# Kernel tuning notes

Hardware: AMD Instinct MI355X
Metric: run time of the kernel (lower is better)

Reference implementation:

```python
import jax, jax.numpy as jnp
import numpy as np
from jax import lax

B, CIN, COUT, K, L = 128, 8, 64, 33, 4096
STRIDE, PAD = 1, 16
HID, NW = 128, 3  # agent hidden, num wavelet types (morlet, mexhat, laplace)
MEXHAT_NORM = 2.0 / (np.sqrt(3.0) * np.pi ** 0.25)


def setup_inputs() -> dict:
    key = jax.random.key(0)
    ks = jax.random.split(key, 12)
    s = 0.05  # small init scale for agent weights
    return {
        "x": jax.random.normal(ks[0], (B, CIN, L), jnp.float32),
        # torch init: ones; add small noise so per-wavelet scales differ
        "superparams": jnp.ones((COUT, CIN, NW), jnp.float32)
        + 0.1 * jax.random.normal(ks[1], (COUT, CIN, NW), jnp.float32),
        "threshold": jnp.full((COUT,), 0.1, jnp.float32),
        "fw": s * jax.random.normal(ks[2], (2 * CIN, HID), jnp.float32),
        "fb": jnp.zeros((HID,), jnp.float32),
        "vw1": s * jax.random.normal(ks[3], (HID, HID), jnp.float32),
        "vb1": jnp.zeros((HID,), jnp.float32),
        "vw2": s * jax.random.normal(ks[4], (HID, 1), jnp.float32),
        "vb2": jnp.zeros((1,), jnp.float32),
        "aw1": s * jax.random.normal(ks[5], (HID, HID), jnp.float32),
        "ab1": jnp.zeros((HID,), jnp.float32),
        "aw2": s * jax.random.normal(ks[6], (HID, NW), jnp.float32),
        "ab2": jnp.zeros((NW,), jnp.float32),
    }


def _softplus_pos(p):
    return jax.nn.softplus(p) + 1e-6


def _make_kernels(superparams):
    # superparams: [COUT, CIN, NW] -> kernel bank [NW, COUT, CIN, K]
    grid = jnp.arange(-(K // 2), K // 2 + 1, dtype=jnp.float32)  # [K]
    scale = _softplus_pos(superparams)  # [COUT, CIN, NW]
    kernels = []
    for i, name in enumerate(("morlet", "mexhat", "laplace")):
        xi = grid[None, None, :] / scale[:, :, i : i + 1]  # [COUT, CIN, K]
        if name == "morlet":
            ker = jnp.exp(-0.5 * xi * xi) * jnp.cos(5.0 * xi)
        elif name == "mexhat":
            ker = MEXHAT_NORM * (1.0 - xi * xi) * jnp.exp(-0.5 * xi * xi)
        else:  # laplace
            ker = jnp.sign(grid)[None, None, :] * jnp.exp(-jnp.abs(xi))
        ker = ker - ker.mean(axis=-1, keepdims=True)
        ker = ker / (jnp.linalg.norm(ker, axis=-1, keepdims=True) + 1e-6)
        kernels.append(ker)
    return jnp.stack(kernels, axis=0)  # [NW, COUT, CIN, K]


def _q_values(states, fw, fb, vw1, vb1, vw2, vb2, aw1, ab1, aw2, ab2):
    h = jax.nn.relu(states @ fw + fb)                     # [B, HID]
    v = jax.nn.relu(h @ vw1 + vb1) @ vw2 + vb2            # [B, 1]
    a = jax.nn.relu(h @ aw1 + ab1) @ aw2 + ab2            # [B, NW]
    return v + a - a.mean(axis=1, keepdims=True)


def reference(x, superparams, threshold, fw, fb, vw1, vb1, vw2, vb2,
              aw1, ab1, aw2, ab2):
    # RL state: per-channel mean & (unbiased) std of the signal -> [B, 2*CIN]
    states = jnp.concatenate([x.mean(axis=-1), x.std(axis=-1, ddof=1)], axis=1)
    q = _q_values(states, fw, fb, vw1, vb1, vw2, vb2, aw1, ab1, aw2, ab2)
    actions = jnp.argmax(q, axis=1)                        # [B], greedy (eval)

    kernels = _make_kernels(superparams)                   # [NW, COUT, CIN, K]
    w_sel = kernels[actions]                               # [B, COUT, CIN, K]

    def conv_one(xb, wb):  # xb [CIN, L], wb [COUT, CIN, K]
        return lax.conv_general_dilated(
            xb[None], wb, window_strides=(STRIDE,), padding=[(PAD, PAD)],
            dimension_numbers=("NCH", "OIH", "NCH"))[0]

    y = jax.vmap(conv_one)(x, w_sel)                       # [B, COUT, Lout]

    # soft shrinkage (denoising) with strictly positive learnable threshold
    tau = _softplus_pos(threshold)[None, :, None]
    return jnp.sign(y) * jnp.maximum(jnp.abs(y) - tau, 0.0)
```

## Files before the change

### kernel.cpp

```cpp
#include <hip/hip_runtime.h>
#include <hip/hip_bf16.h>
#include <cmath>

#define B     128
#define CIN   8
#define COUT  64
#define K     33
#define KP    36
#define KKD   (KP * CIN)
#define NSL   (KKD / 32)
#define L     4096
#define PAD   16
#define HID   128
#define NW    3

#define TL    1024
#define NROW  (TL + KP)
#define OSTR  40

typedef __attribute__((ext_vector_type(8))) short short8;
typedef __attribute__((ext_vector_type(4))) float f32x4;

__device__ __forceinline__ float softplusf(float v) {
    return (v > 20.f) ? v : log1pf(expf(v));
}

__global__ __launch_bounds__(256) void prologue_kernel(
    const float* __restrict__ x,
    const float* __restrict__ fw, const float* __restrict__ fb,
    const float* __restrict__ aw1, const float* __restrict__ ab1,
    const float* __restrict__ aw2, const float* __restrict__ ab2,
    const float* __restrict__ sp,
    int* __restrict__ actions, __hip_bfloat16* __restrict__ bankbf)
{
    const int tid = threadIdx.x;

    if (blockIdx.x < B) {
        const int b = blockIdx.x;
        __shared__ float st[2 * CIN];
        __shared__ float h[HID];
        __shared__ float ha[HID];

        const int ci  = tid >> 5;
        const int sub = tid & 31;
        const float* xp = x + ((size_t)b * CIN + ci) * L;
        float s = 0.f, ss = 0.f;
        for (int j = sub; j < L / 4; j += 32) {
            float4 v = ((const float4*)xp)[j];
            s  += v.x + v.y + v.z + v.w;
            ss += v.x * v.x + v.y * v.y + v.z * v.z + v.w * v.w;
        }
        for (int m = 16; m; m >>= 1) {
            s  += __shfl_xor(s,  m);
            ss += __shfl_xor(ss, m);
        }
        if (sub == 0) {
            float mean = s / (float)L;
            float var  = fmaxf(ss - s * mean, 0.f) / (float)(L - 1);
            st[ci]       = mean;
            st[CIN + ci] = sqrtf(var);
        }
        __syncthreads();

        const int j = tid;
        if (j < HID) {
            float acc = fb[j];
            #pragma unroll
            for (int i = 0; i < 2 * CIN; ++i) acc = fmaf(st[i], fw[i * HID + j], acc);
            h[j] = fmaxf(acc, 0.f);
        }
        __syncthreads();
        if (j < HID) {
            float acc2 = ab1[j];
            for (int i = 0; i < HID; ++i) acc2 = fmaf(h[i], aw1[i * HID + j], acc2);
            ha[j] = fmaxf(acc2, 0.f);
        }
        __syncthreads();
        if (j == 0) {
            float best = -1e30f; int bi = 0;
            for (int w = 0; w < NW; ++w) {
                float a = ab2[w];
                for (int i = 0; i < HID; ++i) a = fmaf(ha[i], aw2[i * NW + w], a);
                if (a > best) { best = a; bi = w; }
            }
            actions[b] = bi;
        }
    } else {
        const int t = (blockIdx.x - B) * 256 + tid;
        if (t >= NW * COUT * CIN) return;
        const int nw = t >> 9;
        const int co = (t >> 3) & 63;
        const int ci = t & 7;

        const float p = sp[(co * CIN + ci) * NW + nw];
        const float scale = softplusf(p) + 1e-6f;

        float ker[K];
        float mean = 0.f;
        #pragma unroll
        for (int k = 0; k < K; ++k) {
            float g  = (float)(k - K / 2);
            float xi = g / scale;
            float v;
            if (nw == 0) {
                v = expf(-0.5f * xi * xi) * cosf(5.f * xi);
            } else if (nw == 1) {
                v = 0.8673250705840776f * (1.f - xi * xi) * expf(-0.5f * xi * xi);
            } else {
                float sgn = (g > 0.f) ? 1.f : ((g < 0.f) ? -1.f : 0.f);
                v = sgn * expf(-fabsf(xi));
            }
            ker[k] = v; mean += v;
        }
        mean *= (1.f / (float)K);
        float nrm = 0.f;
        #pragma unroll
        for (int k = 0; k < K; ++k) { ker[k] -= mean; nrm += ker[k] * ker[k]; }
        const float inv = 1.f / (sqrtf(nrm) + 1e-6f);

        __hip_bfloat16* dst = bankbf + ((size_t)(nw * COUT + co)) * KKD + ci;
        #pragma unroll
        for (int k = 0; k < K; ++k) dst[k * CIN] = __float2bfloat16(ker[k] * inv);
        #pragma unroll
        for (int k = K; k < KP; ++k) dst[k * CIN] = __float2bfloat16(0.f);
    }
}

__global__ __launch_bounds__(512, 4) void conv_kernel(
    const float* __restrict__ x, const __hip_bfloat16* __restrict__ bankbf,
    const int* __restrict__ actions, const float* __restrict__ threshold,
    float* __restrict__ out)
{
    const int b  = blockIdx.y;
    const int l0 = blockIdx.x * TL;
    const int tid  = threadIdx.x;
    const int lane = tid & 63;
    const int w    = tid >> 6;
    const int p    = w & 1;
    const int q    = w >> 1;
    const int g    = lane >> 4;
    const int ln   = lane & 15;

    __shared__ short8 xT[NROW];
    __shared__ float  obuf[8][32 * OSTR];

    {
        __hip_bfloat16* xb = (__hip_bfloat16*)xT;
        for (int idx = tid; idx < CIN * (NROW / 4); idx += 512) {
            int ci = idx / (NROW / 4);
            int r4 = (idx - ci * (NROW / 4)) * 4;
            int gp = l0 - PAD + r4;
            const float* xp = x + ((size_t)b * CIN + ci) * L;
            if (gp >= 0 && gp <= L - 4) {
                float4 v = *(const float4*)&xp[gp];
                xb[(r4 + 0) * CIN + ci] = __float2bfloat16(v.x);
                xb[(r4 + 1) * CIN + ci] = __float2bfloat16(v.y);
                xb[(r4 + 2) * CIN + ci] = __float2bfloat16(v.z);
                xb[(r4 + 3) * CIN + ci] = __float2bfloat16(v.w);
            } else {
                #pragma unroll
                for (int e = 0; e < 4; ++e) {
                    int gpe = gp + e;
                    float f = (gpe >= 0 && gpe < L) ? xp[gpe] : 0.f;
                    xb[(r4 + e) * CIN + ci] = __float2bfloat16(f);
                }
            }
        }
    }

    const int act = __builtin_amdgcn_readfirstlane(actions[b]);
    const short8* wq = (const short8*)(bankbf + (size_t)act * COUT * KKD);
    short8 aQ[2][NSL];
    #pragma unroll
    for (int cc = 0; cc < 2; ++cc) {
        const short8* wrow = wq + ((2 * p + cc) * 16 + ln) * (KKD / 8);
        #pragma unroll
        for (int s = 0; s < NSL; ++s) aQ[cc][s] = wrow[4 * s + g];
    }

    float tau[2];
    #pragma unroll
    for (int cc = 0; cc < 2; ++cc)
        tau[cc] = softplusf(threshold[(2 * p + cc) * 16 + ln]) + 1e-6f;

    const int co_r = lane >> 3;
    const int lc   = lane & 7;

    __syncthreads();

    const int wl0 = q * (TL / 4);
    for (int lt = 0; lt < (TL / 4) / 32; ++lt) {
        const int lbase = wl0 + lt * 32;
        const int r0    = lbase + ln + g;
        f32x4 acc[2][2] = {{{0.f,0.f,0.f,0.f},{0.f,0.f,0.f,0.f}},
                           {{0.f,0.f,0.f,0.f},{0.f,0.f,0.f,0.f}}};
        #pragma unroll
        for (int s = 0; s < NSL; ++s) {
            short8 bf0 = xT[r0 + 4 * s];
            short8 bf1 = xT[r0 + 16 + 4 * s];
            acc[0][0] = __builtin_amdgcn_mfma_f32_16x16x32_bf16(bf0, aQ[0][s], acc[0][0], 0, 0, 0);
            acc[1][0] = __builtin_amdgcn_mfma_f32_16x16x32_bf16(bf0, aQ[1][s], acc[1][0], 0, 0, 0);
            acc[0][1] = __builtin_amdgcn_mfma_f32_16x16x32_bf16(bf1, aQ[0][s], acc[0][1], 0, 0, 0);
            acc[1][1] = __builtin_amdgcn_mfma_f32_16x16x32_bf16(bf1, aQ[1][s], acc[1][1], 0, 0, 0);
        }

        #pragma unroll
        for (int cc = 0; cc < 2; ++cc) {
            #pragma unroll
            for (int sub = 0; sub < 2; ++sub) {
                f32x4 a = acc[cc][sub];
                f32x4 o;
                o[0] = copysignf(fmaxf(fabsf(a[0]) - tau[cc], 0.f), a[0]);
                o[1] = copysignf(fmaxf(fabsf(a[1]) - tau[cc], 0.f), a[1]);
                o[2] = copysignf(fmaxf(fabsf(a[2]) - tau[cc], 0.f), a[2]);
                o[3] = copysignf(fmaxf(fabsf(a[3]) - tau[cc], 0.f), a[3]);
                *(f32x4*)&obuf[w][(cc * 16 + ln) * OSTR + 16 * sub + 4 * g] = o;
            }
        }

        #pragma unroll
        for (int i = 0; i < 4; ++i) {
            const int col = co_r + 8 * i;
            f32x4 v = *(const f32x4*)&obuf[w][col * OSTR + 4 * lc];
            const int co = (2 * p + (col >> 4)) * 16 + (col & 15);
            *(f32x4*)&out[((size_t)b * COUT + co) * L + l0 + lbase + 4 * lc] = v;
        }
    }
}

extern "C" void kernel_launch(void* const* d_in, const int* in_sizes, int n_in,
                              void* d_out, int out_size, void* d_ws, size_t ws_size,
                              hipStream_t stream)
{
    const float* x           = (const float*)d_in[0];
    const float* superparams = (const float*)d_in[1];
    const float* threshold   = (const float*)d_in[2];
    const float* fw          = (const float*)d_in[3];
    const float* fb          = (const float*)d_in[4];
    const float* aw1         = (const float*)d_in[9];
    const float* ab1         = (const float*)d_in[10];
    const float* aw2         = (const float*)d_in[11];
    const float* ab2         = (const float*)d_in[12];
    float* out = (float*)d_out;

    int* actions            = (int*)d_ws;
    __hip_bfloat16* bankbf  = (__hip_bfloat16*)((char*)d_ws + 1024);

    prologue_kernel<<<B + 6, 256, 0, stream>>>(
        x, fw, fb, aw1, ab1, aw2, ab2, superparams, actions, bankbf);
    conv_kernel<<<dim3(L / TL, B), 512, 0, stream>>>(
        x, bankbf, actions, threshold, out);
}
```

Measured before the change: 197.9 us.

## Precompute bf16 channel-interleaved input in a wide stats/cast pass

Adds a statcast kernel spread over 1024 blocks. It computes per-slice channel sums and squared sums and writes x as padded bf16 rows with 8 channels interleaved into a workspace buffer. A separate kernel reduces the partial sums and runs the MLP and the kernel-bank build. The conv kernel then copies the pre-transposed bf16 rows straight into shared memory, replacing its strided fp32 load and transpose. This removes the serial per-batch stats pass and the costly LDS scatter, at the price of an extra launch and an extra write and read of a bf16 copy of x. If the workspace is too small, the old two-kernel path is used instead.

```diff
diff --git a/kernel.cpp b/kernel.cpp
--- a/kernel.cpp
+++ b/kernel.cpp
@@ -17,12 +17,167 @@
 #define TL    1024
 #define NROW  (TL + KP)
 #define OSTR  40
+#define XROWS (PAD + L + KP)
 
 typedef __attribute__((ext_vector_type(8))) short short8;
 typedef __attribute__((ext_vector_type(4))) float f32x4;
 
 __device__ __forceinline__ float softplusf(float v) {
     return (v > 20.f) ? v : log1pf(expf(v));
+}
+__device__ __forceinline__ short f2bf(float f) {
+    __hip_bfloat16 h = __float2bfloat16(f);
+    return *reinterpret_cast<short*>(&h);
+}
+
+__global__ __launch_bounds__(256) void statcast_kernel(
+    const float* __restrict__ x, __hip_bfloat16* __restrict__ xg,
+    float* __restrict__ psum)
+{
+    const int bid = blockIdx.x;
+    const int b  = bid >> 3;
+    const int ls = bid & 7;
+    const int tid  = threadIdx.x;
+    const int lane = tid & 63;
+    const int wv   = tid >> 6;
+    const int l    = ls * 512 + 2 * tid;
+
+    float2 v[CIN];
+    float s[CIN], q[CIN];
+    #pragma unroll
+    for (int ci = 0; ci < CIN; ++ci) {
+        v[ci] = *(const float2*)&x[((size_t)b * CIN + ci) * L + l];
+        s[ci] = v[ci].x + v[ci].y;
+        q[ci] = v[ci].x * v[ci].x + v[ci].y * v[ci].y;
+    }
+
+    short8 ra, rb;
+    #pragma unroll
+    for (int ci = 0; ci < CIN; ++ci) {
+        ra[ci] = f2bf(v[ci].x);
+        rb[ci] = f2bf(v[ci].y);
+    }
+    short8* xr = (short8*)xg + (size_t)b * XROWS + PAD + l;
+    xr[0] = ra;
+    xr[1] = rb;
+
+    short8 z8 = {0,0,0,0,0,0,0,0};
+    if (ls == 0 && tid < PAD) ((short8*)xg)[(size_t)b * XROWS + tid] = z8;
+    if (ls == 7 && tid < KP)  ((short8*)xg)[(size_t)b * XROWS + PAD + L + tid] = z8;
+
+    #pragma unroll
+    for (int m = 32; m; m >>= 1) {
+        #pragma unroll
+        for (int ci = 0; ci < CIN; ++ci) {
+            s[ci] += __shfl_xor(s[ci], m);
+            q[ci] += __shfl_xor(q[ci], m);
+        }
+    }
+    __shared__ float rs[4][CIN], rq[4][CIN];
+    if (lane == 0) {
+        #pragma unroll
+        for (int ci = 0; ci < CIN; ++ci) { rs[wv][ci] = s[ci]; rq[wv][ci] = q[ci]; }
+    }
+    __syncthreads();
+    if (tid < CIN) {
+        float S = rs[0][tid] + rs[1][tid] + rs[2][tid] + rs[3][tid];
+        float Q = rq[0][tid] + rq[1][tid] + rq[2][tid] + rq[3][tid];
+        psum[bid * CIN + tid]             = S;
+        psum[B * 64 + bid * CIN + tid]    = Q;
+    }
+}
+
+__global__ __launch_bounds__(256) void mlpbank_kernel(
+    const float* __restrict__ psum,
+    const float* __restrict__ fw, const float* __restrict__ fb,
+    const float* __restrict__ aw1, const float* __restrict__ ab1,
+    const float* __restrict__ aw2, const float* __restrict__ ab2,
+    const float* __restrict__ sp,
+    int* __restrict__ actions, __hip_bfloat16* __restrict__ bankbf)
+{
+    const int tid = threadIdx.x;
+
+    if (blockIdx.x < B) {
+        const int b = blockIdx.x;
+        __shared__ float st[2 * CIN];
+        __shared__ float h[HID];
+        __shared__ float ha[HID];
+
+        if (tid < CIN) {
+            float S = 0.f, Q = 0.f;
+            #pragma unroll
+            for (int ls = 0; ls < 8; ++ls) {
+                S += psum[(b * 8 + ls) * CIN + tid];
+                Q += psum[B * 64 + (b * 8 + ls) * CIN + tid];
+            }
+            float mean = S / (float)L;
+            float var  = fmaxf(Q - S * mean, 0.f) / (float)(L - 1);
+            st[tid]       = mean;
+            st[CIN + tid] = sqrtf(var);
+        }
+        __syncthreads();
+
+        if (tid < HID) {
+            float acc = fb[tid];
+            #pragma unroll
+            for (int i = 0; i < 2 * CIN; ++i) acc = fmaf(st[i], fw[i * HID + tid], acc);
+            h[tid] = fmaxf(acc, 0.f);
+        }
+        __syncthreads();
+        if (tid < HID) {
+            float acc2 = ab1[tid];
+            for (int i = 0; i < HID; ++i) acc2 = fmaf(h[i], aw1[i * HID + tid], acc2);
+            ha[tid] = fmaxf(acc2, 0.f);
+        }
+        __syncthreads();
+        if (tid == 0) {
+            float best = -1e30f; int bi = 0;
+            for (int w = 0; w < NW; ++w) {
+                float a = ab2[w];
+                for (int i = 0; i < HID; ++i) a = fmaf(ha[i], aw2[i * NW + w], a);
+                if (a > best) { best = a; bi = w; }
+            }
+            actions[b] = bi;
+        }
+    } else {
+        const int t = (blockIdx.x - B) * 256 + tid;
+        if (t >= NW * COUT * CIN) return;
+        const int nw = t >> 9;
+        const int co = (t >> 3) & 63;
+        const int ci = t & 7;
+
+        const float p = sp[(co * CIN + ci) * NW + nw];
+        const float scale = softplusf(p) + 1e-6f;
+
+        float ker[K];
+        float mean = 0.f;
+        #pragma unroll
+        for (int k = 0; k < K; ++k) {
+            float g  = (float)(k - K / 2);
+            float xi = g / scale;
+            float vv;
+            if (nw == 0) {
+                vv = expf(-0.5f * xi * xi) * cosf(5.f * xi);
+            } else if (nw == 1) {
+                vv = 0.8673250705840776f * (1.f - xi * xi) * expf(-0.5f * xi * xi);
+            } else {
+                float sgn = (g > 0.f) ? 1.f : ((g < 0.f) ? -1.f : 0.f);
+                vv = sgn * expf(-fabsf(xi));
+            }
+            ker[k] = vv; mean += vv;
+        }
+        mean *= (1.f / (float)K);
+        float nrm = 0.f;
+        #pragma unroll
+        for (int k = 0; k < K; ++k) { ker[k] -= mean; nrm += ker[k] * ker[k]; }
+        const float inv = 1.f / (sqrtf(nrm) + 1e-6f);
+
+        __hip_bfloat16* dst = bankbf + ((size_t)(nw * COUT + co)) * KKD + ci;
+        #pragma unroll
+        for (int k = 0; k < K; ++k) dst[k * CIN] = __float2bfloat16(ker[k] * inv);
+        #pragma unroll
+        for (int k = K; k < KP; ++k) dst[k * CIN] = __float2bfloat16(0.f);
+    }
 }
 
 __global__ __launch_bounds__(256) void prologue_kernel(
@@ -62,21 +217,20 @@
         }
         __syncthreads();
 
-        const int j = tid;
-        if (j < HID) {
-            float acc = fb[j];
+        if (tid < HID) {
+            float acc = fb[tid];
             #pragma unroll
-            for (int i = 0; i < 2 * CIN; ++i) acc = fmaf(st[i], fw[i * HID + j], acc);
-            h[j] = fmaxf(acc, 0.f);
-        }
-        __syncthreads();
-        if (j < HID) {
-            float acc2 = ab1[j];
-            for (int i = 0; i < HID; ++i) acc2 = fmaf(h[i], aw1[i * HID + j], acc2);
-            ha[j] = fmaxf(acc2, 0.f);
-        }
-        __syncthreads();
-        if (j == 0) {
+            for (int i = 0; i < 2 * CIN; ++i) acc = fmaf(st[i], fw[i * HID + tid], acc);
+            h[tid] = fmaxf(acc, 0.f);
+        }
+        __syncthreads();
+        if (tid < HID) {
+            float acc2 = ab1[tid];
+            for (int i = 0; i < HID; ++i) acc2 = fmaf(h[i], aw1[i * HID + tid], acc2);
+            ha[tid] = fmaxf(acc2, 0.f);
+        }
+        __syncthreads();
+        if (tid == 0) {
             float best = -1e30f; int bi = 0;
             for (int w = 0; w < NW; ++w) {
                 float a = ab2[w];
@@ -101,16 +255,16 @@
         for (int k = 0; k < K; ++k) {
             float g  = (float)(k - K / 2);
             float xi = g / scale;
-            float v;
+            float vv;
             if (nw == 0) {
-                v = expf(-0.5f * xi * xi) * cosf(5.f * xi);
+                vv = expf(-0.5f * xi * xi) * cosf(5.f * xi);
             } else if (nw == 1) {
-                v = 0.8673250705840776f * (1.f - xi * xi) * expf(-0.5f * xi * xi);
+                vv = 0.8673250705840776f * (1.f - xi * xi) * expf(-0.5f * xi * xi);
             } else {
                 float sgn = (g > 0.f) ? 1.f : ((g < 0.f) ? -1.f : 0.f);
-                v = sgn * expf(-fabsf(xi));
-            }
-            ker[k] = v; mean += v;
+                vv = sgn * expf(-fabsf(xi));
+            }
+            ker[k] = vv; mean += vv;
         }
         mean *= (1.f / (float)K);
         float nrm = 0.f;
@@ -126,8 +280,10 @@
     }
 }
 
+template<int XGPATH>
 __global__ __launch_bounds__(512, 4) void conv_kernel(
-    const float* __restrict__ x, const __hip_bfloat16* __restrict__ bankbf,
+    const float* __restrict__ x, const __hip_bfloat16* __restrict__ xg,
+    const __hip_bfloat16* __restrict__ bankbf,
     const int* __restrict__ actions, const float* __restrict__ threshold,
     float* __restrict__ out)
 {
@@ -144,7 +300,10 @@
     __shared__ short8 xT[NROW];
     __shared__ float  obuf[8][32 * OSTR];
 
-    {
+    if constexpr (XGPATH) {
+        const short8* xr = (const short8*)xg + (size_t)b * XROWS + l0;
+        for (int r = tid; r < NROW; r += 512) xT[r] = xr[r];
+    } else {
         __hip_bfloat16* xb = (__hip_bfloat16*)xT;
         for (int idx = tid; idx < CIN * (NROW / 4); idx += 512) {
             int ci = idx / (NROW / 4);
@@ -243,11 +402,22 @@
     const float* ab2         = (const float*)d_in[12];
     float* out = (float*)d_out;
 
-    int* actions            = (int*)d_ws;
-    __hip_bfloat16* bankbf  = (__hip_bfloat16*)((char*)d_ws + 1024);
-
-    prologue_kernel<<<B + 6, 256, 0, stream>>>(
-        x, fw, fb, aw1, ab1, aw2, ab2, superparams, actions, bankbf);
-    conv_kernel<<<dim3(L / TL, B), 512, 0, stream>>>(
-        x, bankbf, actions, threshold, out);
-}
+    int*            actions = (int*)d_ws;
+    float*          psum    = (float*)((char*)d_ws + 4096);
+    __hip_bfloat16* bankbf  = (__hip_bfloat16*)((char*)d_ws + 81920);
+    __hip_bfloat16* xg      = (__hip_bfloat16*)((char*)d_ws + 262144);
+    const size_t needed = 262144 + (size_t)B * XROWS * CIN * 2;
+
+    if (ws_size >= needed) {
+        statcast_kernel<<<B * 8, 256, 0, stream>>>(x, xg, psum);
+        mlpbank_kernel<<<B + 6, 256, 0, stream>>>(
+            psum, fw, fb, aw1, ab1, aw2, ab2, superparams, actions, bankbf);
+        conv_kernel<1><<<dim3(L / TL, B), 512, 0, stream>>>(
+            x, xg, bankbf, actions, threshold, out);
+    } else {
+        prologue_kernel<<<B + 6, 256, 0, stream>>>(
+            x, fw, fb, aw1, ab1, aw2, ab2, superparams, actions, bankbf);
+        conv_kernel<0><<<dim3(L / TL, B), 512, 0, stream>>>(
+            x, xg, bankbf, actions, threshold, out);
+    }
+}
```

After: 194.9 us, median of 2. Within noise of the previous version (-1.5%).
